# Kernel optimization log

Hardware: AMD Instinct MI355X
Metric: run time of the kernel (lower is better)

## Reference

```python
import jax, jax.numpy as jnp
import numpy as np

B, S, D, H, HID = 2, 2048, 256, 8, 1024
EPS = 1e-9


def gelu_fast(x):
    return 0.5 * x * (1.0 + jnp.tanh(x * 0.7978845608 * (1.0 + 0.044715 * x * x)))


def layer_norm(x, g, b):
    m = jnp.mean(x, axis=-1, keepdims=True)
    v = jnp.mean(jnp.square(x - m), axis=-1, keepdims=True)
    return (x - m) * jax.lax.rsqrt(v + EPS) * g + b


def setup_inputs() -> dict:
    key = jax.random.key(0)
    ks = jax.random.split(key, 16)
    x = jax.random.normal(ks[0], (B, S, D), dtype=jnp.float32)
    # causal look-ahead mask: additive, 0 on/below diagonal, -1e9 above
    causal = jnp.triu(jnp.ones((S, S), dtype=jnp.float32), k=1) * (-1e9)
    look_ahead_mask = causal[None, None, :, :]  # (1,1,S,S)
    sd = 0.02
    return {
        "x": x,
        "look_ahead_mask": look_ahead_mask,
        "ln1_g": jnp.ones((D,), jnp.float32),
        "ln1_b": jnp.zeros((D,), jnp.float32),
        "wq_w": jax.random.normal(ks[1], (D * H, D), jnp.float32) * sd,
        "wq_b": jnp.zeros((D * H,), jnp.float32),
        "wk_w": jax.random.normal(ks[2], (D * H, D), jnp.float32) * sd,
        "wk_b": jnp.zeros((D * H,), jnp.float32),
        "wv_w": jax.random.normal(ks[3], (D * H, D), jnp.float32) * sd,
        "wv_b": jnp.zeros((D * H,), jnp.float32),
        "dense_w": jax.random.normal(ks[4], (D, D * H), jnp.float32) * sd,
        "dense_b": jnp.zeros((D,), jnp.float32),
        "ln2_g": jnp.ones((D,), jnp.float32),
        "ln2_b": jnp.zeros((D,), jnp.float32),
        "fc1_w": jax.random.normal(ks[5], (HID, D), jnp.float32) * sd,
        "fc1_b": jnp.zeros((HID,), jnp.float32),
        "fc2_w": jax.random.normal(ks[6], (D, HID), jnp.float32) * sd,
        "fc2_b": jnp.zeros((D,), jnp.float32),
    }


def reference(x, look_ahead_mask, ln1_g, ln1_b, wq_w, wq_b, wk_w, wk_b,
              wv_w, wv_b, dense_w, dense_b, ln2_g, ln2_b,
              fc1_w, fc1_b, fc2_w, fc2_b):
    xn = layer_norm(x, ln1_g, ln1_b)
    # QKV: D -> D*H, each head has full head-dim D (module quirk)
    q = (jnp.einsum('bsd,ed->bse', xn, wq_w) + wq_b).reshape(B, S, H, D).transpose(0, 2, 1, 3)
    k = (jnp.einsum('bsd,ed->bse', xn, wk_w) + wk_b).reshape(B, S, H, D).transpose(0, 2, 1, 3)
    v = (jnp.einsum('bsd,ed->bse', xn, wv_w) + wv_b).reshape(B, S, H, D).transpose(0, 2, 1, 3)
    scores = jnp.einsum('bhqd,bhkd->bhqk', q, k) / jnp.sqrt(jnp.float32(D))
    scores = scores + look_ahead_mask
    attn_weights = jax.nn.softmax(scores, axis=-1)
    ctx = jnp.einsum('bhqk,bhkd->bhqd', attn_weights, v)  # (B,H,S,D)
    ctx = ctx.transpose(0, 2, 1, 3).reshape(B, S, H * D)
    attn = jnp.einsum('bse,de->bsd', ctx, dense_w) + dense_b
    x1 = xn + attn  # residual uses post-LN x (module quirk)
    m = layer_norm(x1, ln2_g, ln2_b)
    m = gelu_fast(jnp.einsum('bsd,hd->bsh', m, fc1_w) + fc1_b)
    m = jnp.einsum('bsh,dh->bsd', m, fc2_w) + fc2_b
    out = x1 + m
    return out, attn_weights
```

## Files before the change

### kernel.cpp

```cpp
#include <hip/hip_runtime.h>
#include <hip/hip_bf16.h>


typedef __bf16 bf16_t;
typedef __bf16 bf16x8 __attribute__((ext_vector_type(8)));
typedef __bf16 bf16x4 __attribute__((ext_vector_type(4)));
typedef float  f32x4  __attribute__((ext_vector_type(4)));

#define DEV __device__ __forceinline__

DEV f32x4 mfma16(bf16x8 a, bf16x8 b, f32x4 c) {
  return __builtin_amdgcn_mfma_f32_16x16x32_bf16(a, b, c, 0, 0, 0);
}

DEV void gload16(const void* g, void* l) {
  __builtin_amdgcn_global_load_lds(
      (const __attribute__((address_space(1))) unsigned int*)g,
      (__attribute__((address_space(3))) unsigned int*)l, 16, 0, 0);
}

__global__ __launch_bounds__(256) void cvt_all(
    const float* __restrict__ s0, const float* __restrict__ s1,
    const float* __restrict__ s2, const float* __restrict__ s3,
    const float* __restrict__ s4, const float* __restrict__ s5,
    bf16_t* __restrict__ d0, bf16_t* __restrict__ d1, bf16_t* __restrict__ d2,
    bf16_t* __restrict__ d3, bf16_t* __restrict__ d4, bf16_t* __restrict__ d5) {
  int i = blockIdx.x * 256 + threadIdx.x;
  const float* s; bf16_t* d; int off;
  if      (i < 131072) { s = s0; d = d0; off = i; }
  else if (i < 262144) { s = s1; d = d1; off = i - 131072; }
  else if (i < 393216) { s = s2; d = d2; off = i - 262144; }
  else if (i < 524288) { s = s3; d = d3; off = i - 393216; }
  else if (i < 589824) { s = s4; d = d4; off = i - 524288; }
  else                 { s = s5; d = d5; off = i - 589824; }
  float4 v = ((const float4*)s)[off];
  bf16x4 o = { (bf16_t)v.x, (bf16_t)v.y, (bf16_t)v.z, (bf16_t)v.w };
  ((bf16x4*)d)[off] = o;
}

__global__ __launch_bounds__(256) void ln_k(const float* __restrict__ x,
    const float* __restrict__ g, const float* __restrict__ bta,
    float* __restrict__ of, bf16_t* __restrict__ ob) {
  int row = blockIdx.x * 4 + (threadIdx.x >> 6);
  int l = threadIdx.x & 63;
  const float4 v = *(const float4*)(x + (size_t)row * 256 + l * 4);
  float s  = v.x + v.y + v.z + v.w;
  float s2 = v.x*v.x + v.y*v.y + v.z*v.z + v.w*v.w;
#pragma unroll
  for (int o = 1; o < 64; o <<= 1) { s += __shfl_xor(s, o, 64); s2 += __shfl_xor(s2, o, 64); }
  float m   = s * (1.f/256.f);
  float var = s2 * (1.f/256.f) - m * m;
  float rs  = rsqrtf(var + 1e-9f);
  const float4 gv = *(const float4*)(g   + l * 4);
  const float4 bv = *(const float4*)(bta + l * 4);
  float4 y;
  y.x = (v.x - m) * rs * gv.x + bv.x;
  y.y = (v.y - m) * rs * gv.y + bv.y;
  y.z = (v.z - m) * rs * gv.z + bv.z;
  y.w = (v.w - m) * rs * gv.w + bv.w;
  if (of) *(float4*)(of + (size_t)row * 256 + l * 4) = y;
  bf16x4 yb = { (bf16_t)y.x, (bf16_t)y.y, (bf16_t)y.z, (bf16_t)y.w };
  *(bf16x4*)(ob + (size_t)row * 256 + l * 4) = yb;
}

DEV void gemm_core(const bf16_t* __restrict__ A, const bf16_t* __restrict__ W,
                   int lda, int row0, int col0, int k0, int kiters,
                   char* Asb, char* Bsb, f32x4 (&acc)[4][4]) {
  int tid = threadIdx.x, w = tid >> 6, l = tid & 63, l15 = l & 15, lhi = l >> 4;
  int wr = (w >> 1) * 64, wc = (w & 1) * 64;

#define STAGE(buf, kk) do {                                                   \
    char* Ad = Asb + (buf) * 8192 + w * 1024;                                 \
    char* Bd = Bsb + (buf) * 8192 + w * 1024;                                 \
    _Pragma("unroll")                                                         \
    for (int j = 0; j < 2; ++j) {                                             \
      int idx = (j * 256 + tid) * 8; int r = idx >> 5, c = idx & 31;          \
      gload16(A + (size_t)(row0 + r) * lda + (kk) + c, Ad + j * 4096);        \
      gload16(W + (size_t)(col0 + r) * lda + (kk) + c, Bd + j * 4096);        \
    } } while (0)

  STAGE(0, k0);
  for (int t = 0; t < kiters; ++t) {
    int cur = t & 1;
    if (t + 1 < kiters) {
      STAGE(cur ^ 1, k0 + (t + 1) * 32);
      asm volatile("s_waitcnt vmcnt(4)" ::: "memory");
    } else {
      asm volatile("s_waitcnt vmcnt(0)" ::: "memory");
    }
    __builtin_amdgcn_s_barrier();
    asm volatile("" ::: "memory");
    const bf16_t* As = (const bf16_t*)(Asb + cur * 8192);
    const bf16_t* Bs = (const bf16_t*)(Bsb + cur * 8192);
    bf16x8 af[4], bfr[4];
#pragma unroll
    for (int m = 0; m < 4; ++m)
      af[m] = *(const bf16x8*)(As + (wr + 16 * m + l15) * 32 + lhi * 8);
#pragma unroll
    for (int n = 0; n < 4; ++n)
      bfr[n] = *(const bf16x8*)(Bs + (wc + 16 * n + l15) * 32 + lhi * 8);
#pragma unroll
    for (int m = 0; m < 4; ++m)
#pragma unroll
      for (int n = 0; n < 4; ++n)
        acc[m][n] = mfma16(af[m], bfr[n], acc[m][n]);
    asm volatile("" ::: "memory");
    __builtin_amdgcn_s_barrier();
  }
#undef STAGE
}

__global__ __launch_bounds__(256, 2) void gemm_qkv(
    const bf16_t* __restrict__ A,
    const bf16_t* __restrict__ W0, const bf16_t* __restrict__ W1, const bf16_t* __restrict__ W2,
    const float* __restrict__ b0, const float* __restrict__ b1, const float* __restrict__ b2,
    bf16_t* __restrict__ qo, bf16_t* __restrict__ ko, bf16_t* __restrict__ vo) {
  __shared__ char Asb[2 * 8192];
  __shared__ char Bsb[2 * 8192];
  int bx = blockIdx.x;
  int wsel = bx >> 4, cb = bx & 15;
  const bf16_t* W    = wsel == 0 ? W0 : (wsel == 1 ? W1 : W2);
  const float*  bias = wsel == 0 ? b0 : (wsel == 1 ? b1 : b2);
  bf16_t*       out  = wsel == 0 ? qo : (wsel == 1 ? ko : vo);
  int row0 = blockIdx.y * 128, col0 = cb * 128;
  f32x4 acc[4][4] = {};
  gemm_core(A, W, 256, row0, col0, 0, 8, Asb, Bsb, acc);

  int tid = threadIdx.x, w = tid >> 6, l = tid & 63, l15 = l & 15, lhi = l >> 4;
  int wr = (w >> 1) * 64, wc = (w & 1) * 64;
#pragma unroll
  for (int m = 0; m < 4; ++m)
#pragma unroll
    for (int n = 0; n < 4; ++n)
#pragma unroll
      for (int j = 0; j < 4; ++j) {
        int row = row0 + wr + 16 * m + lhi * 4 + j;
        int col = col0 + wc + 16 * n + l15;
        float v = acc[m][n][j] + bias[col];
        out[((size_t)((row >> 11) * 8 + (col >> 8)) * 2048 + (row & 2047)) * 256 + (col & 255)] = (bf16_t)v;
      }
}

__global__ __launch_bounds__(256, 2) void gemm_part(
    const bf16_t* __restrict__ A, const bf16_t* __restrict__ W,
    int lda, int ksub, float* __restrict__ parts) {
  __shared__ char Asb[2 * 8192];
  __shared__ char Bsb[2 * 8192];
  int z = blockIdx.z;
  int row0 = blockIdx.y * 128, col0 = blockIdx.x * 128;
  f32x4 acc[4][4] = {};
  gemm_core(A, W, lda, row0, col0, z * ksub, ksub >> 5, Asb, Bsb, acc);

  int tid = threadIdx.x, w = tid >> 6, l = tid & 63, l15 = l & 15, lhi = l >> 4;
  int wr = (w >> 1) * 64, wc = (w & 1) * 64;
  float* p = parts + (size_t)z * 1048576;
#pragma unroll
  for (int m = 0; m < 4; ++m)
#pragma unroll
    for (int n = 0; n < 4; ++n)
#pragma unroll
      for (int j = 0; j < 4; ++j) {
        int row = row0 + wr + 16 * m + lhi * 4 + j;
        int col = col0 + wc + 16 * n + l15;
        p[(size_t)row * 256 + col] = acc[m][n][j];
      }
}

__global__ __launch_bounds__(256) void reduce4(
    const float* __restrict__ parts, const float* __restrict__ bias,
    const float* __restrict__ res, float* __restrict__ out) {
  int i = blockIdx.x * 256 + threadIdx.x;
  f32x4 s = *(const f32x4*)(parts + (size_t)i * 4);
  s += *(const f32x4*)(parts + 1048576 + (size_t)i * 4);
  s += *(const f32x4*)(parts + 2097152 + (size_t)i * 4);
  s += *(const f32x4*)(parts + 3145728 + (size_t)i * 4);
  s += *(const f32x4*)(res + (size_t)i * 4);
  s += *(const f32x4*)(bias + (i & 63) * 4);
  *(f32x4*)(out + (size_t)i * 4) = s;
}

__global__ __launch_bounds__(256, 2) void gemm_fc1(
    const bf16_t* __restrict__ A, const bf16_t* __restrict__ W,
    const float* __restrict__ bias, bf16_t* __restrict__ out) {
  __shared__ char Asb[2 * 8192];
  __shared__ char Bsb[2 * 8192];
  int row0 = blockIdx.y * 128, col0 = blockIdx.x * 128;
  f32x4 acc[4][4] = {};
  gemm_core(A, W, 256, row0, col0, 0, 8, Asb, Bsb, acc);

  int tid = threadIdx.x, w = tid >> 6, l = tid & 63, l15 = l & 15, lhi = l >> 4;
  int wr = (w >> 1) * 64, wc = (w & 1) * 64;
#pragma unroll
  for (int m = 0; m < 4; ++m)
#pragma unroll
    for (int n = 0; n < 4; ++n)
#pragma unroll
      for (int j = 0; j < 4; ++j) {
        int row = row0 + wr + 16 * m + lhi * 4 + j;
        int col = col0 + wc + 16 * n + l15;
        float t = acc[m][n][j] + bias[col];
        float ge = 0.5f * t * (1.f + tanhf(0.7978845608f * t * (1.f + 0.044715f * t * t)));
        out[(size_t)row * 1024 + col] = (bf16_t)ge;
      }
}

__global__ __launch_bounds__(256) void vtrans(const bf16_t* __restrict__ v, bf16_t* __restrict__ vt) {
  __shared__ bf16_t t[64 * 72];
  int bh = blockIdx.z;
  int s0 = blockIdx.x * 64, d0 = blockIdx.y * 64;
  int tid = threadIdx.x;
#pragma unroll
  for (int j = 0; j < 2; ++j) {
    int cj = j * 256 + tid;
    int r = cj >> 3, c = (cj & 7) * 8;
    *(bf16x8*)(t + r * 72 + c) = *(const bf16x8*)(v + ((size_t)bh * 2048 + s0 + r) * 256 + d0 + c);
  }
  __syncthreads();
#pragma unroll
  for (int j = 0; j < 2; ++j) {
    int cj = j * 256 + tid;
    int rd = cj >> 3, cs = (cj & 7) * 8;
    bf16x8 o;
#pragma unroll
    for (int i = 0; i < 8; ++i) o[i] = t[(cs + i) * 72 + rd];
    *(bf16x8*)(vt + ((size_t)bh * 256 + d0 + rd) * 2048 + s0 + cs) = o;
  }
}

__global__ __launch_bounds__(256, 2) void rowsum_k(
    const bf16_t* __restrict__ qg, const bf16_t* __restrict__ kg,
    float* __restrict__ rsg) {
  __shared__ bf16_t Ksh[2][64 * 256];
  __shared__ float  sl[2][64];
  int bx = blockIdx.x;
  int bh = bx & 15, qt = 31 - (bx >> 4);
  int tid = threadIdx.x, w = tid >> 6, l = tid & 63;
  int l15 = l & 15, lhi = l >> 4;
  int wm = w >> 1, wn = w & 1;
  const bf16_t* Q   = qg + (size_t)bh * 2048 * 256;
  const bf16_t* Kg2 = kg + (size_t)bh * 2048 * 256;
  int qbase = qt * 64;
  int nkt = qt + 1;

  bf16x8 qf[2][8];
#pragma unroll
  for (int m = 0; m < 2; ++m)
#pragma unroll
    for (int ks = 0; ks < 8; ++ks)
      qf[m][ks] = *(const bf16x8*)(Q + (size_t)(qbase + wm * 32 + m * 16 + l15) * 256 + ks * 32 + lhi * 8);

#define RSTAGE(t_) do {                                                        \
    char* dst = (char*)Ksh[(t_) & 1] + w * 1024;                               \
    _Pragma("unroll")                                                          \
    for (int j = 0; j < 8; ++j) {                                              \
      int idx = (j * 256 + tid) * 16; int r = idx >> 9;                        \
      int co = (idx & 511) ^ ((r & 7) << 4);                                   \
      gload16(Kg2 + (size_t)((t_) * 64 + r) * 256 + (co >> 1), dst + j * 4096);\
    } } while (0)

  RSTAGE(0);
  if (nkt > 1) RSTAGE(1);

  float sums[2][4] = {};
  for (int t = 0; t < nkt; ++t) {
    if (t + 1 < nkt) asm volatile("s_waitcnt vmcnt(8)" ::: "memory");
    else             asm volatile("s_waitcnt vmcnt(0)" ::: "memory");
    __builtin_amdgcn_s_barrier();
    const char* Kb = (const char*)Ksh[t & 1];
    f32x4 acc[2][2] = {};
#pragma unroll
    for (int ks = 0; ks < 8; ++ks) {
#pragma unroll
      for (int n2 = 0; n2 < 2; ++n2) {
        int row = wn * 32 + n2 * 16 + l15;
        bf16x8 kb = *(const bf16x8*)(Kb + row * 512 + ((ks * 64 + lhi * 16) ^ ((row & 7) << 4)));
#pragma unroll
        for (int m = 0; m < 2; ++m)
          acc[m][n2] = mfma16(qf[m][ks], kb, acc[m][n2]);
      }
    }
#pragma unroll
    for (int m = 0; m < 2; ++m)
#pragma unroll
      for (int n2 = 0; n2 < 2; ++n2)
#pragma unroll
        for (int j = 0; j < 4; ++j) {
          int qr = qbase + wm * 32 + m * 16 + lhi * 4 + j;
          int kc = t * 64 + wn * 32 + n2 * 16 + l15;
          sums[m][j] += (kc <= qr) ? __expf(acc[m][n2][j] * 0.0625f) : 0.f;
        }
    asm volatile("" ::: "memory");
    __builtin_amdgcn_s_barrier();
    if (t + 2 < nkt) RSTAGE(t + 2);
  }
#undef RSTAGE

#pragma unroll
  for (int m = 0; m < 2; ++m)
#pragma unroll
    for (int j = 0; j < 4; ++j) {
#pragma unroll
      for (int o = 1; o < 16; o <<= 1) sums[m][j] += __shfl_xor(sums[m][j], o, 64);
    }
  if (l15 == 0) {
#pragma unroll
    for (int m = 0; m < 2; ++m)
#pragma unroll
      for (int j = 0; j < 4; ++j)
        sl[wn][wm * 32 + m * 16 + lhi * 4 + j] = sums[m][j];
  }
  __syncthreads();
  if (tid < 64)
    rsg[(size_t)bh * 2048 + qbase + tid] = 1.f / (sl[0][tid] + sl[1][tid]);
}

__global__ __launch_bounds__(256, 2) void attn_pv(
    const bf16_t* __restrict__ qg, const bf16_t* __restrict__ kg,
    const bf16_t* __restrict__ vt, const float* __restrict__ rsg,
    float* __restrict__ pout, bf16_t* __restrict__ ctxo) {
  __shared__ bf16_t Ksh[2][32 * 256];
  __shared__ bf16_t Vsh[2][256 * 32];
  __shared__ bf16_t Psh[64 * 32];
  int bx = blockIdx.x;
  int bh = bx & 15, qt = 31 - (bx >> 4);
  int tid = threadIdx.x, w = tid >> 6, l = tid & 63;
  int l15 = l & 15, lhi = l >> 4;
  int wm = w >> 1, wn = w & 1;
  const bf16_t* Q   = qg + (size_t)bh * 2048 * 256;
  const bf16_t* Kg2 = kg + (size_t)bh * 2048 * 256;
  const bf16_t* Vt  = vt + (size_t)bh * 256 * 2048;
  int qbase = qt * 64;
  int nkt = 2 * (qt + 1);

  bf16x8 qf[2][8];
#pragma unroll
  for (int m = 0; m < 2; ++m)
#pragma unroll
    for (int ks = 0; ks < 8; ++ks)
      qf[m][ks] = *(const bf16x8*)(Q + (size_t)(qbase + wm * 32 + m * 16 + l15) * 256 + ks * 32 + lhi * 8);

  float inv[8];
#pragma unroll
  for (int m = 0; m < 2; ++m)
#pragma unroll
    for (int j = 0; j < 4; ++j)
      inv[m * 4 + j] = rsg[(size_t)bh * 2048 + qbase + wm * 32 + m * 16 + lhi * 4 + j];

#define PSTAGE(t_) do {                                                         \
    char* kd = (char*)Ksh[(t_) & 1] + w * 1024;                                 \
    char* vd = (char*)Vsh[(t_) & 1] + w * 1024;                                 \
    _Pragma("unroll")                                                           \
    for (int j = 0; j < 4; ++j) {                                               \
      int idx = (j * 256 + tid) * 16;                                           \
      { int r = idx >> 9; int co = (idx & 511) ^ ((r & 7) << 4);                \
        gload16(Kg2 + (size_t)((t_) * 32 + r) * 256 + (co >> 1), kd + j * 4096); } \
      { int r = idx >> 6; int co = (idx & 63) ^ (((r >> 2) & 3) << 4);          \
        gload16(Vt + (size_t)r * 2048 + (t_) * 32 + (co >> 1), vd + j * 4096); } \
    } } while (0)

  PSTAGE(0);
  PSTAGE(1);

  f32x4 ctx[4][4] = {};
  for (int t = 0; t < nkt; ++t) {
    if (t + 1 < nkt) asm volatile("s_waitcnt vmcnt(8)" ::: "memory");
    else             asm volatile("s_waitcnt vmcnt(0)" ::: "memory");
    __builtin_amdgcn_s_barrier();
    const char* Kb = (const char*)Ksh[t & 1];
    const char* Vb = (const char*)Vsh[t & 1];

    f32x4 acc[2] = {};
#pragma unroll
    for (int ks = 0; ks < 8; ++ks) {
      int row = wn * 16 + l15;
      bf16x8 kb = *(const bf16x8*)(Kb + row * 512 + ((ks * 64 + lhi * 16) ^ ((row & 7) << 4)));
#pragma unroll
      for (int m = 0; m < 2; ++m)
        acc[m] = mfma16(qf[m][ks], kb, acc[m]);
    }
#pragma unroll
    for (int m = 0; m < 2; ++m)
#pragma unroll
      for (int j = 0; j < 4; ++j) {
        int rr = wm * 32 + m * 16 + lhi * 4 + j;
        int qr = qbase + rr;
        int kc = t * 32 + wn * 16 + l15;
        float e = (kc <= qr) ? __expf(acc[m][j] * 0.0625f) * inv[m * 4 + j] : 0.f;
        int addr = rr * 64 + (wn * 16 + l15) * 2;
        *(bf16_t*)((char*)Psh + (addr ^ (((rr >> 2) & 3) << 4))) = (bf16_t)e;
      }
    asm volatile("" ::: "memory");
    __builtin_amdgcn_s_barrier();

    {
      int row = tid >> 2;
      int ch  = (tid & 3) * 16;
      bf16x8 p8 = *(const bf16x8*)((const char*)Psh + row * 64 + (ch ^ (((row >> 2) & 3) << 4)));
      float* dst = pout + ((size_t)bh * 2048 + qbase + row) * 2048 + t * 32 + (tid & 3) * 8;
      f32x4 lo = { (float)p8[0], (float)p8[1], (float)p8[2], (float)p8[3] };
      f32x4 hi = { (float)p8[4], (float)p8[5], (float)p8[6], (float)p8[7] };
      *(f32x4*)dst = lo;
      *(f32x4*)(dst + 4) = hi;
    }

    bf16x8 pa[4], vb[4];
#pragma unroll
    for (int m4 = 0; m4 < 4; ++m4) {
      int row = m4 * 16 + l15;
      pa[m4] = *(const bf16x8*)((const char*)Psh + ((row * 64 + lhi * 16) ^ (((row >> 2) & 3) << 4)));
    }
#pragma unroll
    for (int n = 0; n < 4; ++n) {
      int row = w * 64 + n * 16 + l15;
      vb[n] = *(const bf16x8*)(Vb + ((row * 64 + lhi * 16) ^ (((row >> 2) & 3) << 4)));
    }
#pragma unroll
    for (int m4 = 0; m4 < 4; ++m4)
#pragma unroll
      for (int n = 0; n < 4; ++n)
        ctx[m4][n] = mfma16(pa[m4], vb[n], ctx[m4][n]);

    asm volatile("" ::: "memory");
    __builtin_amdgcn_s_barrier();
    if (t + 2 < nkt) PSTAGE(t + 2);
  }
#undef PSTAGE

  int b = bh >> 3, h = bh & 7;
#pragma unroll
  for (int m4 = 0; m4 < 4; ++m4)
#pragma unroll
    for (int n = 0; n < 4; ++n)
#pragma unroll
      for (int j = 0; j < 4; ++j) {
        int qr = qbase + m4 * 16 + lhi * 4 + j;
        ctxo[((size_t)b * 2048 + qr) * 2048 + h * 256 + w * 64 + n * 16 + l15] = (bf16_t)ctx[m4][n][j];
      }

  int zs = qbase + 64;
  for (int r = 0; r < 64; ++r) {
    size_t base = ((size_t)bh * 2048 + qbase + r) * 2048;
    for (int c = zs + tid * 4; c < 2048; c += 1024) {
      *(float4*)(pout + base + c) = make_float4(0.f, 0.f, 0.f, 0.f);
    }
  }
}

extern "C" void kernel_launch(void* const* d_in, const int* in_sizes, int n_in,
                              void* d_out, int out_size, void* d_ws, size_t ws_size,
                              hipStream_t stream) {
  const float* x     = (const float*)d_in[0];
  const float* ln1g  = (const float*)d_in[2];
  const float* ln1b  = (const float*)d_in[3];
  const float* wq_w  = (const float*)d_in[4];
  const float* wq_b  = (const float*)d_in[5];
  const float* wk_w  = (const float*)d_in[6];
  const float* wk_b  = (const float*)d_in[7];
  const float* wv_w  = (const float*)d_in[8];
  const float* wv_b  = (const float*)d_in[9];
  const float* dw    = (const float*)d_in[10];
  const float* db    = (const float*)d_in[11];
  const float* ln2g  = (const float*)d_in[12];
  const float* ln2b  = (const float*)d_in[13];
  const float* f1w   = (const float*)d_in[14];
  const float* f1b   = (const float*)d_in[15];
  const float* f2w   = (const float*)d_in[16];
  const float* f2b   = (const float*)d_in[17];

  char* ws = (char*)d_ws;
  const size_t MB = 1u << 20;
  float*  xn_f = (float*) (ws + 0 * MB);
  bf16_t* xn_b = (bf16_t*)(ws + 4 * MB);
  bf16_t* q_b  = (bf16_t*)(ws + 6 * MB);
  bf16_t* k_b  = (bf16_t*)(ws + 22 * MB);
  bf16_t* v_b  = (bf16_t*)(ws + 38 * MB);
  bf16_t* vt_b = (bf16_t*)(ws + 54 * MB);
  float*  x1_f = (float*) (ws + 70 * MB);
  bf16_t* m_b  = (bf16_t*)(ws + 74 * MB);
  bf16_t* h_b  = (bf16_t*)(ws + 76 * MB);
  bf16_t* wq_bf = (bf16_t*)(ws + 84 * MB);
  bf16_t* wk_bf = wq_bf + 524288;
  bf16_t* wv_bf = wk_bf + 524288;
  bf16_t* dw_bf = wv_bf + 524288;
  bf16_t* f1_bf = dw_bf + 524288;
  bf16_t* f2_bf = f1_bf + 262144;
  float*  rs_f  = (float*)(ws + 90 * MB);
  bf16_t* ctx_b = v_b;
  float* parts_d = (float*)q_b;
  float* parts_f = (float*)k_b;

  float* out0 = (float*)d_out;
  float* pout = out0 + 1048576;

  cvt_all<<<2560, 256, 0, stream>>>(wq_w, wk_w, wv_w, dw, f1w, f2w,
                                    wq_bf, wk_bf, wv_bf, dw_bf, f1_bf, f2_bf);

  ln_k<<<1024, 256, 0, stream>>>(x, ln1g, ln1b, xn_f, xn_b);

  gemm_qkv<<<dim3(48, 32), 256, 0, stream>>>(xn_b, wq_bf, wk_bf, wv_bf,
                                             wq_b, wk_b, wv_b, q_b, k_b, v_b);

  rowsum_k<<<512, 256, 0, stream>>>(q_b, k_b, rs_f);

  vtrans<<<dim3(32, 4, 16), 256, 0, stream>>>(v_b, vt_b);

  attn_pv<<<512, 256, 0, stream>>>(q_b, k_b, vt_b, rs_f, pout, ctx_b);

  gemm_part<<<dim3(2, 32, 4), 256, 0, stream>>>(ctx_b, dw_bf, 2048, 512, parts_d);
  reduce4<<<1024, 256, 0, stream>>>(parts_d, db, xn_f, x1_f);

  ln_k<<<1024, 256, 0, stream>>>(x1_f, ln2g, ln2b, nullptr, m_b);

  gemm_fc1<<<dim3(8, 32), 256, 0, stream>>>(m_b, f1_bf, f1b, h_b);

  gemm_part<<<dim3(2, 32, 4), 256, 0, stream>>>(h_b, f2_bf, 1024, 256, parts_f);
  reduce4<<<1024, 256, 0, stream>>>(parts_f, f2b, x1_f, out0);
}
```

Baseline: 229.5 us.

## Fuse LN with weight conversion, V transpose into QKV epilogue, and reduce with LN2

Merges the first layer norm and weight bf16 conversion into one launch. The V transpose moves into the QKV GEMM epilogue through an LDS staging tile, which removes the separate vtrans kernel and its extra pass over V. The split-K reduction is fused with the second layer norm. It also raises launch_bounds occupancy hints to 4, adds s_setprio around MFMA loops, and waits on lgkmcnt before barriers. Risks are register pressure from the higher occupancy hint and strided V writes from the epilogue.

```diff
diff --git a/kernel.cpp b/kernel.cpp
--- a/kernel.cpp
+++ b/kernel.cpp
@@ -19,48 +19,49 @@
       (__attribute__((address_space(3))) unsigned int*)l, 16, 0, 0);
 }
 
-__global__ __launch_bounds__(256) void cvt_all(
+__global__ __launch_bounds__(256) void k1_lncvt(
+    const float* __restrict__ x, const float* __restrict__ g, const float* __restrict__ bta,
+    float* __restrict__ of, bf16_t* __restrict__ ob,
     const float* __restrict__ s0, const float* __restrict__ s1,
     const float* __restrict__ s2, const float* __restrict__ s3,
     const float* __restrict__ s4, const float* __restrict__ s5,
     bf16_t* __restrict__ d0, bf16_t* __restrict__ d1, bf16_t* __restrict__ d2,
     bf16_t* __restrict__ d3, bf16_t* __restrict__ d4, bf16_t* __restrict__ d5) {
-  int i = blockIdx.x * 256 + threadIdx.x;
-  const float* s; bf16_t* d; int off;
-  if      (i < 131072) { s = s0; d = d0; off = i; }
-  else if (i < 262144) { s = s1; d = d1; off = i - 131072; }
-  else if (i < 393216) { s = s2; d = d2; off = i - 262144; }
-  else if (i < 524288) { s = s3; d = d3; off = i - 393216; }
-  else if (i < 589824) { s = s4; d = d4; off = i - 524288; }
-  else                 { s = s5; d = d5; off = i - 589824; }
-  float4 v = ((const float4*)s)[off];
-  bf16x4 o = { (bf16_t)v.x, (bf16_t)v.y, (bf16_t)v.z, (bf16_t)v.w };
-  ((bf16x4*)d)[off] = o;
-}
-
-__global__ __launch_bounds__(256) void ln_k(const float* __restrict__ x,
-    const float* __restrict__ g, const float* __restrict__ bta,
-    float* __restrict__ of, bf16_t* __restrict__ ob) {
-  int row = blockIdx.x * 4 + (threadIdx.x >> 6);
-  int l = threadIdx.x & 63;
-  const float4 v = *(const float4*)(x + (size_t)row * 256 + l * 4);
-  float s  = v.x + v.y + v.z + v.w;
-  float s2 = v.x*v.x + v.y*v.y + v.z*v.z + v.w*v.w;
-#pragma unroll
-  for (int o = 1; o < 64; o <<= 1) { s += __shfl_xor(s, o, 64); s2 += __shfl_xor(s2, o, 64); }
-  float m   = s * (1.f/256.f);
-  float var = s2 * (1.f/256.f) - m * m;
-  float rs  = rsqrtf(var + 1e-9f);
-  const float4 gv = *(const float4*)(g   + l * 4);
-  const float4 bv = *(const float4*)(bta + l * 4);
-  float4 y;
-  y.x = (v.x - m) * rs * gv.x + bv.x;
-  y.y = (v.y - m) * rs * gv.y + bv.y;
-  y.z = (v.z - m) * rs * gv.z + bv.z;
-  y.w = (v.w - m) * rs * gv.w + bv.w;
-  if (of) *(float4*)(of + (size_t)row * 256 + l * 4) = y;
-  bf16x4 yb = { (bf16_t)y.x, (bf16_t)y.y, (bf16_t)y.z, (bf16_t)y.w };
-  *(bf16x4*)(ob + (size_t)row * 256 + l * 4) = yb;
+  int bid = blockIdx.x;
+  if (bid < 1024) {
+    int row = bid * 4 + (threadIdx.x >> 6);
+    int l = threadIdx.x & 63;
+    const float4 v = *(const float4*)(x + (size_t)row * 256 + l * 4);
+    float s  = v.x + v.y + v.z + v.w;
+    float s2 = v.x*v.x + v.y*v.y + v.z*v.z + v.w*v.w;
+#pragma unroll
+    for (int o = 1; o < 64; o <<= 1) { s += __shfl_xor(s, o, 64); s2 += __shfl_xor(s2, o, 64); }
+    float m   = s * (1.f/256.f);
+    float var = s2 * (1.f/256.f) - m * m;
+    float rs  = rsqrtf(var + 1e-9f);
+    const float4 gv = *(const float4*)(g   + l * 4);
+    const float4 bv = *(const float4*)(bta + l * 4);
+    float4 y;
+    y.x = (v.x - m) * rs * gv.x + bv.x;
+    y.y = (v.y - m) * rs * gv.y + bv.y;
+    y.z = (v.z - m) * rs * gv.z + bv.z;
+    y.w = (v.w - m) * rs * gv.w + bv.w;
+    *(float4*)(of + (size_t)row * 256 + l * 4) = y;
+    bf16x4 yb = { (bf16_t)y.x, (bf16_t)y.y, (bf16_t)y.z, (bf16_t)y.w };
+    *(bf16x4*)(ob + (size_t)row * 256 + l * 4) = yb;
+  } else {
+    int i = (bid - 1024) * 256 + threadIdx.x;
+    const float* s; bf16_t* d; int off;
+    if      (i < 131072) { s = s0; d = d0; off = i; }
+    else if (i < 262144) { s = s1; d = d1; off = i - 131072; }
+    else if (i < 393216) { s = s2; d = d2; off = i - 262144; }
+    else if (i < 524288) { s = s3; d = d3; off = i - 393216; }
+    else if (i < 589824) { s = s4; d = d4; off = i - 524288; }
+    else                 { s = s5; d = d5; off = i - 589824; }
+    float4 v = ((const float4*)s)[off];
+    bf16x4 o = { (bf16_t)v.x, (bf16_t)v.y, (bf16_t)v.z, (bf16_t)v.w };
+    ((bf16x4*)d)[off] = o;
+  }
 }
 
 DEV void gemm_core(const bf16_t* __restrict__ A, const bf16_t* __restrict__ W,
@@ -104,44 +105,72 @@
 #pragma unroll
       for (int n = 0; n < 4; ++n)
         acc[m][n] = mfma16(af[m], bfr[n], acc[m][n]);
-    asm volatile("" ::: "memory");
+    asm volatile("s_waitcnt lgkmcnt(0)" ::: "memory");
     __builtin_amdgcn_s_barrier();
   }
 #undef STAGE
 }
 
-__global__ __launch_bounds__(256, 2) void gemm_qkv(
+__global__ __launch_bounds__(256, 4) void gemm_qkv(
     const bf16_t* __restrict__ A,
     const bf16_t* __restrict__ W0, const bf16_t* __restrict__ W1, const bf16_t* __restrict__ W2,
     const float* __restrict__ b0, const float* __restrict__ b1, const float* __restrict__ b2,
-    bf16_t* __restrict__ qo, bf16_t* __restrict__ ko, bf16_t* __restrict__ vo) {
-  __shared__ char Asb[2 * 8192];
-  __shared__ char Bsb[2 * 8192];
+    bf16_t* __restrict__ qo, bf16_t* __restrict__ ko, bf16_t* __restrict__ vto) {
+  __shared__ char smem[34816];
+  char* Asb = smem;
+  char* Bsb = smem + 16384;
   int bx = blockIdx.x;
   int wsel = bx >> 4, cb = bx & 15;
   const bf16_t* W    = wsel == 0 ? W0 : (wsel == 1 ? W1 : W2);
   const float*  bias = wsel == 0 ? b0 : (wsel == 1 ? b1 : b2);
-  bf16_t*       out  = wsel == 0 ? qo : (wsel == 1 ? ko : vo);
   int row0 = blockIdx.y * 128, col0 = cb * 128;
   f32x4 acc[4][4] = {};
   gemm_core(A, W, 256, row0, col0, 0, 8, Asb, Bsb, acc);
 
   int tid = threadIdx.x, w = tid >> 6, l = tid & 63, l15 = l & 15, lhi = l >> 4;
   int wr = (w >> 1) * 64, wc = (w & 1) * 64;
-#pragma unroll
-  for (int m = 0; m < 4; ++m)
-#pragma unroll
-    for (int n = 0; n < 4; ++n)
-#pragma unroll
-      for (int j = 0; j < 4; ++j) {
-        int row = row0 + wr + 16 * m + lhi * 4 + j;
-        int col = col0 + wc + 16 * n + l15;
-        float v = acc[m][n][j] + bias[col];
-        out[((size_t)((row >> 11) * 8 + (col >> 8)) * 2048 + (row & 2047)) * 256 + (col & 255)] = (bf16_t)v;
+
+  if (wsel < 2) {
+    bf16_t* out = wsel == 0 ? qo : ko;
+#pragma unroll
+    for (int m = 0; m < 4; ++m)
+#pragma unroll
+      for (int n = 0; n < 4; ++n)
+#pragma unroll
+        for (int j = 0; j < 4; ++j) {
+          int row = row0 + wr + 16 * m + lhi * 4 + j;
+          int col = col0 + wc + 16 * n + l15;
+          float v = acc[m][n][j] + bias[col];
+          out[((size_t)((row >> 11) * 8 + (col >> 8)) * 2048 + (row & 2047)) * 256 + (col & 255)] = (bf16_t)v;
+        }
+  } else {
+    __syncthreads();
+    bf16_t* T = (bf16_t*)smem;
+#pragma unroll
+    for (int m = 0; m < 4; ++m)
+#pragma unroll
+      for (int n = 0; n < 4; ++n) {
+        int d = wc + 16 * n + l15;
+        int s = wr + 16 * m + lhi * 4;
+        bf16x4 v4;
+#pragma unroll
+        for (int j = 0; j < 4; ++j) v4[j] = (bf16_t)(acc[m][n][j] + bias[col0 + d]);
+        *(bf16x4*)(T + d * 136 + s) = v4;
       }
-}
-
-__global__ __launch_bounds__(256, 2) void gemm_part(
+    __syncthreads();
+    int bh = ((row0 >> 11) << 3) + (col0 >> 8);
+    int d0 = col0 & 255, s0g = row0 & 2047;
+#pragma unroll
+    for (int p = 0; p < 8; ++p) {
+      int idx = p * 256 + tid;
+      int d = idx >> 4, c = (idx & 15) * 8;
+      bf16x8 v8 = *(const bf16x8*)(T + d * 136 + c);
+      *(bf16x8*)(vto + ((size_t)bh * 256 + d0 + d) * 2048 + s0g + c) = v8;
+    }
+  }
+}
+
+__global__ __launch_bounds__(256, 4) void gemm_part(
     const bf16_t* __restrict__ A, const bf16_t* __restrict__ W,
     int lda, int ksub, float* __restrict__ parts) {
   __shared__ char Asb[2 * 8192];
@@ -179,7 +208,38 @@
   *(f32x4*)(out + (size_t)i * 4) = s;
 }
 
-__global__ __launch_bounds__(256, 2) void gemm_fc1(
+__global__ __launch_bounds__(256) void reduce_ln(
+    const float* __restrict__ parts, const float* __restrict__ bias,
+    const float* __restrict__ res, const float* __restrict__ g,
+    const float* __restrict__ bta, float* __restrict__ x1o, bf16_t* __restrict__ mo) {
+  int row = blockIdx.x * 4 + (threadIdx.x >> 6);
+  int l = threadIdx.x & 63;
+  size_t base = (size_t)row * 256 + l * 4;
+  f32x4 s = *(const f32x4*)(parts + base);
+  s += *(const f32x4*)(parts + 1048576 + base);
+  s += *(const f32x4*)(parts + 2097152 + base);
+  s += *(const f32x4*)(parts + 3145728 + base);
+  s += *(const f32x4*)(res + base);
+  s += *(const f32x4*)(bias + l * 4);
+  *(f32x4*)(x1o + base) = s;
+  float sm = s[0] + s[1] + s[2] + s[3];
+  float s2 = s[0]*s[0] + s[1]*s[1] + s[2]*s[2] + s[3]*s[3];
+#pragma unroll
+  for (int o = 1; o < 64; o <<= 1) { sm += __shfl_xor(sm, o, 64); s2 += __shfl_xor(s2, o, 64); }
+  float m   = sm * (1.f/256.f);
+  float var = s2 * (1.f/256.f) - m * m;
+  float rs  = rsqrtf(var + 1e-9f);
+  const float4 gv = *(const float4*)(g   + l * 4);
+  const float4 bv = *(const float4*)(bta + l * 4);
+  bf16x4 yb;
+  yb[0] = (bf16_t)((s[0] - m) * rs * gv.x + bv.x);
+  yb[1] = (bf16_t)((s[1] - m) * rs * gv.y + bv.y);
+  yb[2] = (bf16_t)((s[2] - m) * rs * gv.z + bv.z);
+  yb[3] = (bf16_t)((s[3] - m) * rs * gv.w + bv.w);
+  *(bf16x4*)(mo + base) = yb;
+}
+
+__global__ __launch_bounds__(256, 4) void gemm_fc1(
     const bf16_t* __restrict__ A, const bf16_t* __restrict__ W,
     const float* __restrict__ bias, bf16_t* __restrict__ out) {
   __shared__ char Asb[2 * 8192];
@@ -202,29 +262,6 @@
         float ge = 0.5f * t * (1.f + tanhf(0.7978845608f * t * (1.f + 0.044715f * t * t)));
         out[(size_t)row * 1024 + col] = (bf16_t)ge;
       }
-}
-
-__global__ __launch_bounds__(256) void vtrans(const bf16_t* __restrict__ v, bf16_t* __restrict__ vt) {
-  __shared__ bf16_t t[64 * 72];
-  int bh = blockIdx.z;
-  int s0 = blockIdx.x * 64, d0 = blockIdx.y * 64;
-  int tid = threadIdx.x;
-#pragma unroll
-  for (int j = 0; j < 2; ++j) {
-    int cj = j * 256 + tid;
-    int r = cj >> 3, c = (cj & 7) * 8;
-    *(bf16x8*)(t + r * 72 + c) = *(const bf16x8*)(v + ((size_t)bh * 2048 + s0 + r) * 256 + d0 + c);
-  }
-  __syncthreads();
-#pragma unroll
-  for (int j = 0; j < 2; ++j) {
-    int cj = j * 256 + tid;
-    int rd = cj >> 3, cs = (cj & 7) * 8;
-    bf16x8 o;
-#pragma unroll
-    for (int i = 0; i < 8; ++i) o[i] = t[(cs + i) * 72 + rd];
-    *(bf16x8*)(vt + ((size_t)bh * 256 + d0 + rd) * 2048 + s0 + cs) = o;
-  }
 }
 
 __global__ __launch_bounds__(256, 2) void rowsum_k(
@@ -268,6 +305,7 @@
     __builtin_amdgcn_s_barrier();
     const char* Kb = (const char*)Ksh[t & 1];
     f32x4 acc[2][2] = {};
+    __builtin_amdgcn_s_setprio(1);
 #pragma unroll
     for (int ks = 0; ks < 8; ++ks) {
 #pragma unroll
@@ -279,6 +317,7 @@
           acc[m][n2] = mfma16(qf[m][ks], kb, acc[m][n2]);
       }
     }
+    __builtin_amdgcn_s_setprio(0);
 #pragma unroll
     for (int m = 0; m < 2; ++m)
 #pragma unroll
@@ -289,7 +328,7 @@
           int kc = t * 64 + wn * 32 + n2 * 16 + l15;
           sums[m][j] += (kc <= qr) ? __expf(acc[m][n2][j] * 0.0625f) : 0.f;
         }
-    asm volatile("" ::: "memory");
+    asm volatile("s_waitcnt lgkmcnt(0)" ::: "memory");
     __builtin_amdgcn_s_barrier();
     if (t + 2 < nkt) RSTAGE(t + 2);
   }
@@ -370,6 +409,7 @@
     const char* Vb = (const char*)Vsh[t & 1];
 
     f32x4 acc[2] = {};
+    __builtin_amdgcn_s_setprio(1);
 #pragma unroll
     for (int ks = 0; ks < 8; ++ks) {
       int row = wn * 16 + l15;
@@ -378,6 +418,7 @@
       for (int m = 0; m < 2; ++m)
         acc[m] = mfma16(qf[m][ks], kb, acc[m]);
     }
+    __builtin_amdgcn_s_setprio(0);
 #pragma unroll
     for (int m = 0; m < 2; ++m)
 #pragma unroll
@@ -389,7 +430,7 @@
         int addr = rr * 64 + (wn * 16 + l15) * 2;
         *(bf16_t*)((char*)Psh + (addr ^ (((rr >> 2) & 3) << 4))) = (bf16_t)e;
       }
-    asm volatile("" ::: "memory");
+    asm volatile("s_waitcnt lgkmcnt(0)" ::: "memory");
     __builtin_amdgcn_s_barrier();
 
     {
@@ -414,13 +455,15 @@
       int row = w * 64 + n * 16 + l15;
       vb[n] = *(const bf16x8*)(Vb + ((row * 64 + lhi * 16) ^ (((row >> 2) & 3) << 4)));
     }
+    __builtin_amdgcn_s_setprio(1);
 #pragma unroll
     for (int m4 = 0; m4 < 4; ++m4)
 #pragma unroll
       for (int n = 0; n < 4; ++n)
         ctx[m4][n] = mfma16(pa[m4], vb[n], ctx[m4][n]);
-
-    asm volatile("" ::: "memory");
+    __builtin_amdgcn_s_setprio(0);
+
+    asm volatile("s_waitcnt lgkmcnt(0)" ::: "memory");
     __builtin_amdgcn_s_barrier();
     if (t + 2 < nkt) PSTAGE(t + 2);
   }
@@ -473,7 +516,7 @@
   bf16_t* xn_b = (bf16_t*)(ws + 4 * MB);
   bf16_t* q_b  = (bf16_t*)(ws + 6 * MB);
   bf16_t* k_b  = (bf16_t*)(ws + 22 * MB);
-  bf16_t* v_b  = (bf16_t*)(ws + 38 * MB);
+  bf16_t* ctx_b= (bf16_t*)(ws + 38 * MB);
   bf16_t* vt_b = (bf16_t*)(ws + 54 * MB);
   float*  x1_f = (float*) (ws + 70 * MB);
   bf16_t* m_b  = (bf16_t*)(ws + 74 * MB);
@@ -485,31 +528,25 @@
   bf16_t* f1_bf = dw_bf + 524288;
   bf16_t* f2_bf = f1_bf + 262144;
   float*  rs_f  = (float*)(ws + 90 * MB);
-  bf16_t* ctx_b = v_b;
   float* parts_d = (float*)q_b;
   float* parts_f = (float*)k_b;
 
   float* out0 = (float*)d_out;
   float* pout = out0 + 1048576;
 
-  cvt_all<<<2560, 256, 0, stream>>>(wq_w, wk_w, wv_w, dw, f1w, f2w,
-                                    wq_bf, wk_bf, wv_bf, dw_bf, f1_bf, f2_bf);
-
-  ln_k<<<1024, 256, 0, stream>>>(x, ln1g, ln1b, xn_f, xn_b);
+  k1_lncvt<<<3584, 256, 0, stream>>>(x, ln1g, ln1b, xn_f, xn_b,
+                                     wq_w, wk_w, wv_w, dw, f1w, f2w,
+                                     wq_bf, wk_bf, wv_bf, dw_bf, f1_bf, f2_bf);
 
   gemm_qkv<<<dim3(48, 32), 256, 0, stream>>>(xn_b, wq_bf, wk_bf, wv_bf,
-                                             wq_b, wk_b, wv_b, q_b, k_b, v_b);
+                                             wq_b, wk_b, wv_b, q_b, k_b, vt_b);
 
   rowsum_k<<<512, 256, 0, stream>>>(q_b, k_b, rs_f);
 
-  vtrans<<<dim3(32, 4, 16), 256, 0, stream>>>(v_b, vt_b);
-
   attn_pv<<<512, 256, 0, stream>>>(q_b, k_b, vt_b, rs_f, pout, ctx_b);
 
   gemm_part<<<dim3(2, 32, 4), 256, 0, stream>>>(ctx_b, dw_bf, 2048, 512, parts_d);
-  reduce4<<<1024, 256, 0, stream>>>(parts_d, db, xn_f, x1_f);
-
-  ln_k<<<1024, 256, 0, stream>>>(x1_f, ln2g, ln2b, nullptr, m_b);
+  reduce_ln<<<1024, 256, 0, stream>>>(parts_d, db, xn_f, ln2g, ln2b, x1_f, m_b);
 
   gemm_fc1<<<dim3(8, 32), 256, 0, stream>>>(m_b, f1_bf, f1b, h_b);
 
```

Result: faster. 217.5 us (-5.2%).
